# Kernel optimization log

Hardware: AMD Instinct MI355X
Metric: run time of the kernel (lower is better)

The kernel has to match this reference:

```python
import jax, jax.numpy as jnp
import numpy as np

B, N, C_IN, C_OUT = 128, 512, 64, 64
ALPHA = 0.2  # LeakyReLU negative slope
NEG_INF = -9e15


def setup_inputs() -> dict:
    key = jax.random.key(0)
    k_x, k_adj, k_W, k_a, k_b = jax.random.split(key, 5)
    x = jax.random.normal(k_x, (B, N, C_IN), dtype=jnp.float32)
    adj = jax.random.randint(k_adj, (N, N), 0, 2, dtype=jnp.int32)
    # Xavier-uniform-ish init for W:[2,C_IN,C_OUT] and a:[2*C_OUT,1]
    limW = 1.414 * np.sqrt(6.0 / (C_IN + C_OUT))
    W = jax.random.uniform(k_W, (2, C_IN, C_OUT), jnp.float32, -limW, limW)
    lima = 1.414 * np.sqrt(6.0 / (2 * C_OUT + 1))
    a = jax.random.uniform(k_a, (2 * C_OUT, 1), jnp.float32, -lima, lima)
    stdv = 1.0 / np.sqrt(C_OUT)
    bias = jax.random.uniform(k_b, (C_OUT,), jnp.float32, -stdv, stdv)
    return {"x": x, "adj": adj, "W": W, "a": a, "bias": bias}


def reference(x, adj, W, a, bias):
    F_out = W.shape[2]
    h0 = jnp.einsum('bnc,cf->bnf', x, W[0])
    h1 = jnp.einsum('bnc,cf->bnf', x, W[1])
    h = h0 + h1  # [B,N,F]
    # Separable additive attention score: e[b,i,j] = leaky(a1.h_i + a2.h_j)
    a1 = a[:F_out, 0]
    a2 = a[F_out:, 0]
    s1 = h @ a1  # [B,N]
    s2 = h @ a2  # [B,N]
    e = jax.nn.leaky_relu(s1[:, :, None] + s2[:, None, :], negative_slope=ALPHA)
    att = jnp.where(adj[None, :, :] > 0, e, NEG_INF)
    att = jax.nn.softmax(att, axis=2)  # [B,N,N]
    # attention*M (M=eye) picks diagonal -> route through h0; off-diagonal -> h1
    eye = jnp.eye(att.shape[1], dtype=att.dtype)
    diag = jnp.einsum('bii->bi', att)
    h_prime = diag[:, :, None] * h0 + jnp.einsum('bij,bjf->bif', att * (1.0 - eye), h1)
    return h_prime + bias
```

## Files before the change

### kernel.cpp

```cpp
#include <hip/hip_runtime.h>
#include <hip/hip_bf16.h>

#define BB 128
#define NN 512
#define ALPHA_ 0.2f
#define NEG_INF_ -9.0e15f
#define SPB 536
#define SXW 72

typedef short bf16x8 __attribute__((ext_vector_type(8)));
typedef float f32x4  __attribute__((ext_vector_type(4)));

__device__ __forceinline__ float bfs2f(unsigned short s) {
    unsigned u = ((unsigned)s) << 16;
    return __uint_as_float(u);
}

__global__ __launch_bounds__(256, 4) void k1_proj(
    const float* __restrict__ x, const float* __restrict__ W, const float* __restrict__ a,
    __hip_bfloat16* __restrict__ h1T, __hip_bfloat16* __restrict__ gN,
    float* __restrict__ s1, float* __restrict__ s2)
{
    __shared__ __align__(16) unsigned short sX[64 * SXW];
    __shared__ __align__(16) unsigned short sWb[2][64 * SXW];
    __shared__ unsigned short sT[64 * 66];
    int tid = threadIdx.x, lane = tid & 63, w = tid >> 6;
    int lane15 = lane & 15, quad = lane >> 4;
    int b = blockIdx.x >> 3, n0 = (blockIdx.x & 7) << 6;

    int nl = tid >> 2, q = tid & 3;
    const float* xp = x + ((size_t)b * NN + n0 + nl) * 64 + q * 16;
    float4 v0 = *(const float4*)(xp + 0);
    float4 v1 = *(const float4*)(xp + 4);
    float4 v2 = *(const float4*)(xp + 8);
    float4 v3 = *(const float4*)(xp + 12);

    #pragma unroll
    for (int it = 0; it < 4; ++it) {
        int e  = tid + it * 256;
        int c  = e >> 4;
        int f0 = (e & 15) << 2;
        float4 w0 = *(const float4*)(W + c * 64 + f0);
        float4 w1 = *(const float4*)(W + 4096 + c * 64 + f0);
        __hip_bfloat16 t0;
        t0 = __float2bfloat16(w0.x); sWb[0][(f0 + 0) * SXW + c] = *(unsigned short*)&t0;
        t0 = __float2bfloat16(w0.y); sWb[0][(f0 + 1) * SXW + c] = *(unsigned short*)&t0;
        t0 = __float2bfloat16(w0.z); sWb[0][(f0 + 2) * SXW + c] = *(unsigned short*)&t0;
        t0 = __float2bfloat16(w0.w); sWb[0][(f0 + 3) * SXW + c] = *(unsigned short*)&t0;
        t0 = __float2bfloat16(w1.x); sWb[1][(f0 + 0) * SXW + c] = *(unsigned short*)&t0;
        t0 = __float2bfloat16(w1.y); sWb[1][(f0 + 1) * SXW + c] = *(unsigned short*)&t0;
        t0 = __float2bfloat16(w1.z); sWb[1][(f0 + 2) * SXW + c] = *(unsigned short*)&t0;
        t0 = __float2bfloat16(w1.w); sWb[1][(f0 + 3) * SXW + c] = *(unsigned short*)&t0;
    }
    {
        union { bf16x8 v; __hip_bfloat16 h[8]; } pk0, pk1;
        pk0.h[0]=__float2bfloat16(v0.x); pk0.h[1]=__float2bfloat16(v0.y);
        pk0.h[2]=__float2bfloat16(v0.z); pk0.h[3]=__float2bfloat16(v0.w);
        pk0.h[4]=__float2bfloat16(v1.x); pk0.h[5]=__float2bfloat16(v1.y);
        pk0.h[6]=__float2bfloat16(v1.z); pk0.h[7]=__float2bfloat16(v1.w);
        pk1.h[0]=__float2bfloat16(v2.x); pk1.h[1]=__float2bfloat16(v2.y);
        pk1.h[2]=__float2bfloat16(v2.z); pk1.h[3]=__float2bfloat16(v2.w);
        pk1.h[4]=__float2bfloat16(v3.x); pk1.h[5]=__float2bfloat16(v3.y);
        pk1.h[6]=__float2bfloat16(v3.z); pk1.h[7]=__float2bfloat16(v3.w);
        *(bf16x8*)&sX[nl * SXW + q * 16]     = pk0.v;
        *(bf16x8*)&sX[nl * SXW + q * 16 + 8] = pk1.v;
    }
    __syncthreads();

    f32x4 acc0[4] = {{0,0,0,0},{0,0,0,0},{0,0,0,0},{0,0,0,0}};
    f32x4 acc1[4] = {{0,0,0,0},{0,0,0,0},{0,0,0,0},{0,0,0,0}};
    #pragma unroll
    for (int kt = 0; kt < 2; ++kt) {
        bf16x8 af = *(const bf16x8*)&sX[(w * 16 + lane15) * SXW + kt * 32 + quad * 8];
        #pragma unroll
        for (int nt = 0; nt < 4; ++nt) {
            bf16x8 b0 = *(const bf16x8*)&sWb[0][(nt * 16 + lane15) * SXW + kt * 32 + quad * 8];
            acc0[nt] = __builtin_amdgcn_mfma_f32_16x16x32_bf16(af, b0, acc0[nt], 0, 0, 0);
            bf16x8 b1 = *(const bf16x8*)&sWb[1][(nt * 16 + lane15) * SXW + kt * 32 + quad * 8];
            acc1[nt] = __builtin_amdgcn_mfma_f32_16x16x32_bf16(af, b1, acc1[nt], 0, 0, 0);
        }
    }

    float a1v[4], a2v[4];
    #pragma unroll
    for (int nt = 0; nt < 4; ++nt) {
        a1v[nt] = a[nt * 16 + lane15];
        a2v[nt] = a[64 + nt * 16 + lane15];
    }
    float p1[4] = {0, 0, 0, 0}, p2[4] = {0, 0, 0, 0};
    unsigned short* gNu = (unsigned short*)gN + (size_t)b * 32768 + (size_t)n0 * 64;
    #pragma unroll
    for (int nt = 0; nt < 4; ++nt) {
        #pragma unroll
        for (int r = 0; r < 4; ++r) {
            int nlr = w * 16 + quad * 4 + r;
            int f   = nt * 16 + lane15;
            float h0v = acc0[nt][r], h1v = acc1[nt][r];
            __hip_bfloat16 hb = __float2bfloat16(h1v);
            sT[f * 66 + nlr] = *(unsigned short*)&hb;
            __hip_bfloat16 gb16 = __float2bfloat16(h0v - h1v);
            gNu[(size_t)nlr * 64 + f] = *(unsigned short*)&gb16;
            float hs = h0v + h1v;
            p1[r] = fmaf(hs, a1v[nt], p1[r]);
            p2[r] = fmaf(hs, a2v[nt], p2[r]);
        }
    }
    #pragma unroll
    for (int o = 1; o < 16; o <<= 1) {
        #pragma unroll
        for (int r = 0; r < 4; ++r) {
            p1[r] += __shfl_xor(p1[r], o, 64);
            p2[r] += __shfl_xor(p2[r], o, 64);
        }
    }
    if (lane15 == 0) {
        #pragma unroll
        for (int r = 0; r < 4; ++r) {
            int row = b * NN + n0 + w * 16 + quad * 4 + r;
            s1[row] = p1[r]; s2[row] = p2[r];
        }
    }
    __syncthreads();
    unsigned short* h1Tu = (unsigned short*)h1T;
    #pragma unroll
    for (int fr = 0; fr < 16; ++fr) {
        int f = w * 16 + fr;
        h1Tu[(size_t)b * 32768 + f * 512 + n0 + lane] = sT[f * 66 + lane];
    }
}

__global__ __launch_bounds__(256, 4) void k2_att(
    const int* __restrict__ adj,
    const float* __restrict__ bias,
    const __hip_bfloat16* __restrict__ h1T,
    const __hip_bfloat16* __restrict__ gN,
    const float* __restrict__ s1, const float* __restrict__ s2,
    float* __restrict__ out)
{
    __shared__ __align__(16) __hip_bfloat16 sPb[32 * SPB];
    __shared__ float sInv[32], sPi[32];
    int tid = threadIdx.x, w = tid >> 6, lane = tid & 63;
    int F = blockIdx.x;
    int work = (F & 7) * 256 + (F >> 3);
    int b = work >> 4;
    int i0 = (work & 15) << 5;
    int lane15 = lane & 15, quad = lane >> 4;
    int f = w * 16 + lane15;

    const float* s2b = s2 + (size_t)b * NN;
    float4 q0 = *(const float4*)(s2b + lane * 8);
    float4 q1 = *(const float4*)(s2b + lane * 8 + 4);
    const float* s1p = s1 + (size_t)b * NN + i0 + 8 * w;
    float4 sA = *(const float4*)(s1p + 0);
    float4 sB = *(const float4*)(s1p + 4);
    const unsigned short* gb = (const unsigned short*)gN + (size_t)b * 32768 + f;
    unsigned short gvw[8];
    #pragma unroll
    for (int t = 0; t < 2; ++t)
        #pragma unroll
        for (int r = 0; r < 4; ++r)
            gvw[t * 4 + r] = gb[(size_t)(i0 + t * 16 + quad * 4 + r) * 64];
    const __hip_bfloat16* bptr = h1T + (size_t)b * 32768 + (size_t)f * 512 + quad * 8;
    bf16x8 bfr0[8];
    #pragma unroll
    for (int g = 0; g < 8; ++g)
        bfr0[g] = *(const bf16x8*)(bptr + g * 32);

    float sv[8] = {q0.x, q0.y, q0.z, q0.w, q1.x, q1.y, q1.z, q1.w};
    float s1r[8] = {sA.x, sA.y, sA.z, sA.w, sB.x, sB.y, sB.z, sB.w};

    float ls[8];
    #pragma unroll
    for (int r2 = 0; r2 < 8; ++r2) {
        int r = 8 * w + r2;
        int i = i0 + r;
        float s1i = s1r[r2];
        const int* arow = adj + (size_t)i * NN + lane * 8;
        int4 A0 = *(const int4*)arow;
        int4 A1 = *(const int4*)(arow + 4);
        int av[8] = {A0.x, A0.y, A0.z, A0.w, A1.x, A1.y, A1.z, A1.w};
        float p[8], l = 0.f;
        #pragma unroll
        for (int t = 0; t < 8; ++t) {
            float s = s1i + sv[t];
            s = fmaxf(s, ALPHA_ * s);
            float e = (av[t] > 0) ? s : NEG_INF_;
            p[t] = __expf(e);
            l += p[t];
        }
        ls[r2] = l;
        union { bf16x8 v; __hip_bfloat16 h[8]; } pk;
        #pragma unroll
        for (int t = 0; t < 8; ++t) pk.h[t] = __float2bfloat16(p[t]);
        if (lane == (i >> 3)) sPi[r] = __bfloat162float(pk.h[r2]);
        *(bf16x8*)&sPb[r * SPB + lane * 8] = pk.v;
    }
    #pragma unroll
    for (int o = 32; o > 0; o >>= 1) {
        #pragma unroll
        for (int r2 = 0; r2 < 8; ++r2) ls[r2] += __shfl_xor(ls[r2], o, 64);
    }
    if (lane == 0) {
        #pragma unroll
        for (int r2 = 0; r2 < 8; ++r2) sInv[8 * w + r2] = 1.f / ls[r2];
    }
    __syncthreads();

    const __hip_bfloat16* aptr0 = &sPb[lane15 * SPB + quad * 8];
    const __hip_bfloat16* aptr1 = &sPb[(16 + lane15) * SPB + quad * 8];
    bf16x8 bfr1[8];
    #pragma unroll
    for (int g = 0; g < 8; ++g)
        bfr1[g] = *(const bf16x8*)(bptr + (8 + g) * 32);

    f32x4 acc0 = {0, 0, 0, 0}, acc1 = {0, 0, 0, 0};
    #pragma unroll
    for (int g = 0; g < 8; ++g) {
        bf16x8 a0 = *(const bf16x8*)(aptr0 + g * 32);
        acc0 = __builtin_amdgcn_mfma_f32_16x16x32_bf16(a0, bfr0[g], acc0, 0, 0, 0);
        bf16x8 a1 = *(const bf16x8*)(aptr1 + g * 32);
        acc1 = __builtin_amdgcn_mfma_f32_16x16x32_bf16(a1, bfr0[g], acc1, 0, 0, 0);
    }
    #pragma unroll
    for (int g = 0; g < 8; ++g) {
        int kt = 8 + g;
        bf16x8 a0 = *(const bf16x8*)(aptr0 + kt * 32);
        acc0 = __builtin_amdgcn_mfma_f32_16x16x32_bf16(a0, bfr1[g], acc0, 0, 0, 0);
        bf16x8 a1 = *(const bf16x8*)(aptr1 + kt * 32);
        acc1 = __builtin_amdgcn_mfma_f32_16x16x32_bf16(a1, bfr1[g], acc1, 0, 0, 0);
    }

    float biasf = bias[f];
    #pragma unroll
    for (int t = 0; t < 2; ++t) {
        f32x4 ac = t ? acc1 : acc0;
        #pragma unroll
        for (int r = 0; r < 4; ++r) {
            int m = t * 16 + quad * 4 + r;
            int i = i0 + m;
            float gvf = bfs2f(gvw[t * 4 + r]);
            float inv = sInv[m], pi = sPi[m];
            out[((size_t)b * NN + i) * 64 + f] = (ac[r] + pi * gvf) * inv + biasf;
        }
    }
}

extern "C" void kernel_launch(void* const* d_in, const int* in_sizes, int n_in,
                              void* d_out, int out_size, void* d_ws, size_t ws_size,
                              hipStream_t stream) {
    const void* p_x = nullptr; const void* p_adj = nullptr; const void* p_W = nullptr;
    const void* p_a = nullptr; const void* p_bias = nullptr;
    for (int k = 0; k < n_in; ++k) {
        switch (in_sizes[k]) {
            case 128 * 512 * 64: p_x    = d_in[k]; break;
            case 512 * 512:      p_adj  = d_in[k]; break;
            case 2 * 64 * 64:    p_W    = d_in[k]; break;
            case 2 * 64:         p_a    = d_in[k]; break;
            case 64:             p_bias = d_in[k]; break;
        }
    }
    const float* x    = (const float*)p_x;
    const int*   adj  = (const int*)p_adj;
    const float* W    = (const float*)p_W;
    const float* a    = (const float*)p_a;
    const float* bias = (const float*)p_bias;
    float* out = (float*)d_out;

    __hip_bfloat16* h1T = (__hip_bfloat16*)d_ws;
    __hip_bfloat16* gN  = h1T + 4194304;
    float* s1 = (float*)(gN + 4194304);
    float* s2 = s1 + 65536;

    k1_proj<<<dim3(BB * 8), 256, 0, stream>>>(x, W, a, h1T, gN, s1, s2);
    k2_att<<<dim3(BB * NN / 32), 256, 0, stream>>>(adj, bias, h1T, gN, s1, s2, out);
}
```

Measured before the change: 109.6 us.

## Pack adjacency into bitmask in projection kernel and defer B-fragment loads

```diff
diff --git a/kernel.cpp b/kernel.cpp
--- a/kernel.cpp
+++ b/kernel.cpp
@@ -18,6 +18,7 @@
 
 __global__ __launch_bounds__(256, 4) void k1_proj(
     const float* __restrict__ x, const float* __restrict__ W, const float* __restrict__ a,
+    const int* __restrict__ adj, unsigned char* __restrict__ bits,
     __hip_bfloat16* __restrict__ h1T, __hip_bfloat16* __restrict__ gN,
     float* __restrict__ s1, float* __restrict__ s2)
 {
@@ -34,6 +35,15 @@
     float4 v1 = *(const float4*)(xp + 4);
     float4 v2 = *(const float4*)(xp + 8);
     float4 v3 = *(const float4*)(xp + 12);
+
+    if (tid < 32) {
+        int idx = blockIdx.x * 32 + tid;
+        const int* p = adj + (size_t)idx * 8;
+        unsigned m = 0;
+        #pragma unroll
+        for (int t = 0; t < 8; ++t) m |= (p[t] > 0 ? 1u : 0u) << t;
+        bits[idx] = (unsigned char)m;
+    }
 
     #pragma unroll
     for (int it = 0; it < 4; ++it) {
@@ -130,7 +140,7 @@
 }
 
 __global__ __launch_bounds__(256, 4) void k2_att(
-    const int* __restrict__ adj,
+    const unsigned char* __restrict__ adjbits,
     const float* __restrict__ bias,
     const __hip_bfloat16* __restrict__ h1T,
     const __hip_bfloat16* __restrict__ gN,
@@ -144,29 +154,15 @@
     int work = (F & 7) * 256 + (F >> 3);
     int b = work >> 4;
     int i0 = (work & 15) << 5;
-    int lane15 = lane & 15, quad = lane >> 4;
-    int f = w * 16 + lane15;
 
     const float* s2b = s2 + (size_t)b * NN;
     float4 q0 = *(const float4*)(s2b + lane * 8);
     float4 q1 = *(const float4*)(s2b + lane * 8 + 4);
+    float sv[8] = {q0.x, q0.y, q0.z, q0.w, q1.x, q1.y, q1.z, q1.w};
+
     const float* s1p = s1 + (size_t)b * NN + i0 + 8 * w;
     float4 sA = *(const float4*)(s1p + 0);
     float4 sB = *(const float4*)(s1p + 4);
-    const unsigned short* gb = (const unsigned short*)gN + (size_t)b * 32768 + f;
-    unsigned short gvw[8];
-    #pragma unroll
-    for (int t = 0; t < 2; ++t)
-        #pragma unroll
-        for (int r = 0; r < 4; ++r)
-            gvw[t * 4 + r] = gb[(size_t)(i0 + t * 16 + quad * 4 + r) * 64];
-    const __hip_bfloat16* bptr = h1T + (size_t)b * 32768 + (size_t)f * 512 + quad * 8;
-    bf16x8 bfr0[8];
-    #pragma unroll
-    for (int g = 0; g < 8; ++g)
-        bfr0[g] = *(const bf16x8*)(bptr + g * 32);
-
-    float sv[8] = {q0.x, q0.y, q0.z, q0.w, q1.x, q1.y, q1.z, q1.w};
     float s1r[8] = {sA.x, sA.y, sA.z, sA.w, sB.x, sB.y, sB.z, sB.w};
 
     float ls[8];
@@ -175,16 +171,13 @@
         int r = 8 * w + r2;
         int i = i0 + r;
         float s1i = s1r[r2];
-        const int* arow = adj + (size_t)i * NN + lane * 8;
-        int4 A0 = *(const int4*)arow;
-        int4 A1 = *(const int4*)(arow + 4);
-        int av[8] = {A0.x, A0.y, A0.z, A0.w, A1.x, A1.y, A1.z, A1.w};
+        unsigned mb = adjbits[(size_t)i * 64 + lane];
         float p[8], l = 0.f;
         #pragma unroll
         for (int t = 0; t < 8; ++t) {
             float s = s1i + sv[t];
             s = fmaxf(s, ALPHA_ * s);
-            float e = (av[t] > 0) ? s : NEG_INF_;
+            float e = (mb & (1u << t)) ? s : NEG_INF_;
             p[t] = __expf(e);
             l += p[t];
         }
@@ -206,31 +199,40 @@
     }
     __syncthreads();
 
+    int lane15 = lane & 15, quad = lane >> 4;
+    int n0w = w * 16;
+    int f = n0w + lane15;
+    float biasf = bias[f];
+    const __hip_bfloat16* bptr = h1T + (size_t)b * 32768 + (size_t)f * 512 + quad * 8;
     const __hip_bfloat16* aptr0 = &sPb[lane15 * SPB + quad * 8];
     const __hip_bfloat16* aptr1 = &sPb[(16 + lane15) * SPB + quad * 8];
-    bf16x8 bfr1[8];
-    #pragma unroll
-    for (int g = 0; g < 8; ++g)
-        bfr1[g] = *(const bf16x8*)(bptr + (8 + g) * 32);
+
+    const unsigned short* gb = (const unsigned short*)gN + (size_t)b * 32768 + f;
+    unsigned short gvw[8];
+    #pragma unroll
+    for (int t = 0; t < 2; ++t) {
+        #pragma unroll
+        for (int r = 0; r < 4; ++r)
+            gvw[t * 4 + r] = gb[(size_t)(i0 + t * 16 + quad * 4 + r) * 64];
+    }
 
     f32x4 acc0 = {0, 0, 0, 0}, acc1 = {0, 0, 0, 0};
-    #pragma unroll
-    for (int g = 0; g < 8; ++g) {
-        bf16x8 a0 = *(const bf16x8*)(aptr0 + g * 32);
-        acc0 = __builtin_amdgcn_mfma_f32_16x16x32_bf16(a0, bfr0[g], acc0, 0, 0, 0);
-        bf16x8 a1 = *(const bf16x8*)(aptr1 + g * 32);
-        acc1 = __builtin_amdgcn_mfma_f32_16x16x32_bf16(a1, bfr0[g], acc1, 0, 0, 0);
-    }
-    #pragma unroll
-    for (int g = 0; g < 8; ++g) {
-        int kt = 8 + g;
-        bf16x8 a0 = *(const bf16x8*)(aptr0 + kt * 32);
-        acc0 = __builtin_amdgcn_mfma_f32_16x16x32_bf16(a0, bfr1[g], acc0, 0, 0, 0);
-        bf16x8 a1 = *(const bf16x8*)(aptr1 + kt * 32);
-        acc1 = __builtin_amdgcn_mfma_f32_16x16x32_bf16(a1, bfr1[g], acc1, 0, 0, 0);
-    }
-
-    float biasf = bias[f];
+    bf16x8 bfr[8];
+    #pragma unroll
+    for (int half = 0; half < 2; ++half) {
+        #pragma unroll
+        for (int g = 0; g < 8; ++g)
+            bfr[g] = *(const bf16x8*)(bptr + (half * 8 + g) * 32);
+        #pragma unroll
+        for (int g = 0; g < 8; ++g) {
+            int kt = half * 8 + g;
+            bf16x8 a0 = *(const bf16x8*)(aptr0 + kt * 32);
+            acc0 = __builtin_amdgcn_mfma_f32_16x16x32_bf16(a0, bfr[g], acc0, 0, 0, 0);
+            bf16x8 a1 = *(const bf16x8*)(aptr1 + kt * 32);
+            acc1 = __builtin_amdgcn_mfma_f32_16x16x32_bf16(a1, bfr[g], acc1, 0, 0, 0);
+        }
+    }
+
     #pragma unroll
     for (int t = 0; t < 2; ++t) {
         f32x4 ac = t ? acc1 : acc0;
@@ -240,7 +242,8 @@
             int i = i0 + m;
             float gvf = bfs2f(gvw[t * 4 + r]);
             float inv = sInv[m], pi = sPi[m];
-            out[((size_t)b * NN + i) * 64 + f] = (ac[r] + pi * gvf) * inv + biasf;
+            float v = (ac[r] + pi * gvf) * inv + biasf;
+            __builtin_nontemporal_store(v, &out[((size_t)b * NN + i) * 64 + f]);
         }
     }
 }
@@ -270,7 +273,8 @@
     __hip_bfloat16* gN  = h1T + 4194304;
     float* s1 = (float*)(gN + 4194304);
     float* s2 = s1 + 65536;
-
-    k1_proj<<<dim3(BB * 8), 256, 0, stream>>>(x, W, a, h1T, gN, s1, s2);
-    k2_att<<<dim3(BB * NN / 32), 256, 0, stream>>>(adj, bias, h1T, gN, s1, s2, out);
-}
+    unsigned char* bits = (unsigned char*)(s2 + 65536);
+
+    k1_proj<<<dim3(BB * 8), 256, 0, stream>>>(x, W, a, adj, bits, h1T, gN, s1, s2);
+    k2_att<<<dim3(BB * NN / 32), 256, 0, stream>>>(bits, bias, h1T, gN, s1, s2, out);
+}
```

Measured after the change: 107.0 us. -2.4%, faster.
